# Kernel tuning notes

Hardware: AMD Instinct MI355X
Metric: run time of the kernel (lower is better)

The kernel has to match this reference:

```python
import jax, jax.numpy as jnp
import numpy as np

N_DIMS = 4          # len(dims): gauge-link channels split off by unpack_x
N_BANDS = 3         # SU(3) matrices
THRESHOLD = 1e-3    # trnorm_threshold
LAYER_CH = [6, 12, 12]  # input_channels + args.layer_channels


def cplx_einsum(eq, a, b):
    # complex einsum on real/imag-stacked tensors (last dim = 2)
    ar, ai = a[..., 0], a[..., 1]
    br, bi = b[..., 0], b[..., 1]
    re = jnp.einsum(eq, ar, br) - jnp.einsum(eq, ai, bi)
    im = jnp.einsum(eq, ar, bi) + jnp.einsum(eq, ai, br)
    return jnp.stack((re, im), axis=-1)


def h_conj(w):
    # hermitian conjugate: transpose matrix dims, negate imag part
    wt = jnp.swapaxes(w, -3, -2)
    return jnp.stack((wt[..., 0], -wt[..., 1]), axis=-1)


def gebl(x, weight):
    # x: [b, X, n_dims + n_in, nb, nb, 2]; weight: [n_out, w_in, w_in, 2]
    u, w = x[:, :, :N_DIMS], x[:, :, N_DIMS:]
    w = jnp.concatenate((w, h_conj(w)), axis=2)            # conjugation enlargement
    b, s = w.shape[0], w.shape[1]
    eye = jnp.zeros((N_BANDS, N_BANDS, 2), w.dtype).at[..., 0].set(jnp.eye(N_BANDS, dtype=w.dtype))
    unit = jnp.broadcast_to(eye, (b, s, 1, N_BANDS, N_BANDS, 2))
    w = jnp.concatenate((w, unit), axis=2)                 # unit elements
    ww = cplx_einsum('bxvij,bxwjk->bxvwik', w, w)          # pairwise matrix products
    w_out = cplx_einsum('uvw,bxvwij->bxuij', weight, ww)   # channel mixing
    return jnp.concatenate((u, w_out), axis=2)


def gerelu(x):
    u, w = x[:, :, :N_DIMS], x[:, :, N_DIMS:]
    tr_re = jnp.einsum('bxwiic->bxwc', w)[..., 0]          # Re(Tr W)
    w = jax.nn.relu(tr_re)[..., None, None, None] * w
    return jnp.concatenate((u, w), axis=2)


def trnorm(x):
    # trnorm_on_abs = True branch
    u, w = x[:, :, :N_DIMS], x[:, :, N_DIMS:]
    tr = jnp.einsum('bxviic->bxvc', w)
    tr_abs = jnp.sqrt(tr[..., 0] ** 2 + tr[..., 1] ** 2)
    norm = jnp.maximum(jnp.mean(tr_abs, axis=2), THRESHOLD)
    w = w / norm[:, :, None, None, None, None]
    return jnp.concatenate((u, w), axis=2)


def setup_inputs() -> dict:
    key = jax.random.key(0)
    ks = jax.random.split(key, 5)
    b, X = 2, 8 * 8 * 8 * 8
    x = jax.random.normal(ks[0], (b, X, N_DIMS + LAYER_CH[0], N_BANDS, N_BANDS, 2), jnp.float32)
    # GEBL weights: [n_out, w_in, w_in, 2], w_in = 2*n_in + 1
    w_in1 = 2 * LAYER_CH[0] + 1  # 13
    w_in2 = 2 * LAYER_CH[1] + 1  # 25
    w1 = jax.random.normal(ks[1], (LAYER_CH[1], w_in1, w_in1, 2), jnp.float32) * 0.1
    w2 = jax.random.normal(ks[2], (LAYER_CH[2], w_in2, w_in2, 2), jnp.float32) * 0.1
    dense_w = jax.random.normal(ks[3], (1, LAYER_CH[2] * 2), jnp.float32) * 0.2
    dense_b = jax.random.normal(ks[4], (1,), jnp.float32) * 0.01
    return {"x": x, "w1": w1, "w2": w2, "dense_w": dense_w, "dense_b": dense_b}


def reference(x, w1, w2, dense_w, dense_b):
    # GEBL -> GEReLU -> TrNorm (trnorm_before_ReLU=False), twice
    h = trnorm(gerelu(gebl(x, w1)))
    h = trnorm(gerelu(gebl(h, w2)))
    # Trace (normalized) -> reshape -> dense -> reshape
    w = h[:, :, N_DIMS:]
    tr = (1.0 / N_BANDS) * jnp.einsum('bxwiic->bxwc', w)   # [b, X, c, 2]
    flat = tr.reshape(-1, tr.shape[2] * 2)                 # torch .view: (c,2) interleaved
    out = flat @ dense_w.T + dense_b                        # [b*X, 1]
    return out.reshape(x.shape[0], -1)                      # [b, num_sites]
```

## Files before the change

kernel.cpp:

```cpp
#include <hip/hip_runtime.h>
#include <math.h>


#define NPTS 8192
#define THRESH 0.001f

__global__ void geblnet_setup(const float* __restrict__ w2,
                              float4* __restrict__ CTt) {
    int j = blockIdx.x * blockDim.x + threadIdx.x;
    if (j >= 12 * 169) return;
    int u = j / 169, it = j % 169;
    const float* W = w2 + u * 25 * 25 * 2;
#define WR(v, w) W[((v) * 25 + (w)) * 2]
#define WI(v, w) W[((v) * 25 + (w)) * 2 + 1]
    float c0, c1, c2, c3;
    if (it < 78) {
        int q = it, a = 0;
        while (q >= 12 - a) { q -= 12 - a; ++a; }
        int b = a + q;
        float ar = WR(a, b) + (a != b ? WR(b, a) : 0.f);
        float ai = WI(a, b) + (a != b ? WI(b, a) : 0.f);
        float br = WR(12 + a, 12 + b) + (a != b ? WR(12 + b, 12 + a) : 0.f);
        float bi = WI(12 + a, 12 + b) + (a != b ? WI(12 + b, 12 + a) : 0.f);
        c0 = ar + br; c1 = bi - ai; c2 = ai + bi; c3 = ar - br;
    } else if (it < 156) {
        int q = it - 78, a = 0;
        while (q >= 12 - a) { q -= 12 - a; ++a; }
        int b = a + q;
        if (a != b) {
            float gr = WR(a, 12 + b) + WR(12 + b, a);
            float gi = WI(a, 12 + b) + WI(12 + b, a);
            float dr = WR(b, 12 + a) + WR(12 + a, b);
            float di = WI(b, 12 + a) + WI(12 + a, b);
            c0 = gr + dr; c1 = di - gi; c2 = gi + di; c3 = gr - dr;
        } else {
            float er = WR(a, 12 + a) + WR(12 + a, a);
            float ei = WI(a, 12 + a) + WI(12 + a, a);
            c0 = er; c1 = 0.f; c2 = ei; c3 = 0.f;
        }
    } else if (it < 168) {
        int a = it - 156;
        float fr = WR(a, 24) + WR(24, a), fi = WI(a, 24) + WI(24, a);
        float pr = WR(12 + a, 24) + WR(24, 12 + a);
        float pi = WI(12 + a, 24) + WI(24, 12 + a);
        c0 = fr + pr; c1 = pi - fi; c2 = fi + pi; c3 = fr - pr;
    } else {
        c0 = 3.f * WR(24, 24); c1 = 0.f; c2 = 3.f * WI(24, 24); c3 = 0.f;
    }
    CTt[it * 12 + u] = make_float4(c0, c1, c2, c3);
#undef WR
#undef WI
}

__global__ __launch_bounds__(64) void geblnet_main(
    const float2* __restrict__ x2,
    const float2* __restrict__ w1g,
    const float* __restrict__ dw,
    const float* __restrict__ db,
    const float4* __restrict__ CTt,
    float* __restrict__ out)
{
    __shared__ float2 WeGV[170];
    __shared__ float2 Bs[780];
    __shared__ float2 Hs[108];
    __shared__ float2 Tpar[60];
    __shared__ float2 tr1[12];
    __shared__ float  sc1[12];
    __shared__ float  gb[12];
    __shared__ float  tra[12];

    const int t = threadIdx.x;
    const int p = blockIdx.x;

    for (int j = t; j < 117; j += 64) {
        int v = j / 9, ik = j - v * 9;
        int i = ik / 3, jj = ik - i * 3;
        float2 val;
        if (v < 6) val = x2[(size_t)p * 90 + (4 + v) * 9 + ik];
        else if (v < 12) {
            float2 s = x2[(size_t)p * 90 + (v - 2) * 9 + jj * 3 + i];
            val = make_float2(s.x, -s.y);
        } else val = make_float2((i == jj) ? 1.f : 0.f, 0.f);
        WeGV[v * 10 + ik] = val;
    }
    __syncthreads();

    #pragma unroll 1
    for (int g = 0; g < 2; ++g) {
        const int u0 = g * 6;
        #pragma unroll 1
        for (int e = t; e < 702; e += 64) {
            int uu = e / 117, rem = e - uu * 117;
            int v = rem / 9, jk = rem - v * 9;
            const float2* cp = w1g + ((u0 + uu) * 13 + v) * 13;
            float br = 0.f, bi = 0.f;
            #pragma unroll
            for (int w = 0; w < 13; ++w) {
                float2 cc = cp[w];
                float2 ee = WeGV[w * 10 + jk];
                br += cc.x * ee.x - cc.y * ee.y;
                bi += cc.x * ee.y + cc.y * ee.x;
            }
            Bs[(uu * 13 + v) * 10 + jk] = make_float2(br, bi);
        }
        __syncthreads();
        if (t < 54) {
            int uu = t / 9, ik = t - uu * 9;
            int i = ik / 3, k = ik - i * 3;
            float hr = 0.f, hi = 0.f;
            #pragma unroll
            for (int v = 0; v < 13; ++v) {
                const float2* a = &WeGV[v * 10 + i * 3];
                const float2* b = &Bs[(uu * 13 + v) * 10 + k];
                #pragma unroll
                for (int j = 0; j < 3; ++j) {
                    float2 aj = a[j];
                    float2 bj = b[j * 3];
                    hr += aj.x * bj.x - aj.y * bj.y;
                    hi += aj.x * bj.y + aj.y * bj.x;
                }
            }
            Hs[(u0 + uu) * 9 + ik] = make_float2(hr, hi);
        }
        __syncthreads();
    }

    if (t < 12) {
        float2 a = Hs[t * 9 + 0], b = Hs[t * 9 + 4], c = Hs[t * 9 + 8];
        float2 tt = make_float2(a.x + b.x + c.x, a.y + b.y + c.y);
        tr1[t] = tt;
        float gg = tt.x > 0.f ? tt.x : 0.f;
        gb[t] = gg;
        tra[t] = gg * sqrtf(tt.x * tt.x + tt.y * tt.y);
    }
    __syncthreads();
    if (t < 12) {
        float m = 0.f;
        #pragma unroll
        for (int u = 0; u < 12; ++u) m += tra[u];
        sc1[t] = gb[t] / fmaxf(m * (1.f / 12.f), THRESH);
    }
    __syncthreads();

    for (int it = t; it < 169; it += 64) {
        float2 val;
        if (it < 156) {
            int q = it < 78 ? it : it - 78;
            float fs = sqrtf(625.0f - 8.0f * (float)q);
            int a = (int)((25.0f - fs) * 0.5f);
            int b = q - (a * (25 - a)) / 2 + a;
            const float2* Ha = &Hs[a * 9];
            const float2* Hb = &Hs[b * 9];
            float s = sc1[a] * sc1[b];
            float vr = 0.f, vi = 0.f;
            if (it < 78) {
                #pragma unroll
                for (int i = 0; i < 3; ++i)
                    #pragma unroll
                    for (int jj = 0; jj < 3; ++jj) {
                        float2 A = Ha[i * 3 + jj], B = Hb[jj * 3 + i];
                        vr += A.x * B.x - A.y * B.y;
                        vi += A.x * B.y + A.y * B.x;
                    }
            } else {
                #pragma unroll
                for (int e = 0; e < 9; ++e) {
                    float2 A = Ha[e], B = Hb[e];
                    vr += A.x * B.x + A.y * B.y;
                    vi += A.y * B.x - A.x * B.y;
                }
            }
            val = make_float2(s * vr, s * vi);
        } else if (it < 168) {
            int a = it - 156;
            float s = sc1[a]; float2 tt = tr1[a];
            val = make_float2(s * tt.x, s * tt.y);
        } else {
            val = make_float2(1.f, 0.f);
        }
        WeGV[it] = val;
    }
    __syncthreads();

    if (t < 60) {
        int q = t / 12, u = t - q * 12;
        int i0 = q * 34, i1 = (q == 4) ? 169 : i0 + 34;
        float tre = 0.f, tim = 0.f;
        for (int it = i0; it < i1; ++it) {
            float4 c = CTt[it * 12 + u];
            float2 gv = WeGV[it];
            tre += c.x * gv.x + c.y * gv.y;
            tim += c.z * gv.x + c.w * gv.y;
        }
        Tpar[u * 5 + q] = make_float2(tre, tim);
    }
    __syncthreads();

    if (t < 12) {
        float2 tt = make_float2(0.f, 0.f);
        #pragma unroll
        for (int q = 0; q < 5; ++q) {
            float2 A = Tpar[t * 5 + q];
            tt.x += A.x; tt.y += A.y;
        }
        tr1[t] = tt;
        float g = tt.x > 0.f ? tt.x : 0.f;
        gb[t] = g;
        tra[t] = g * sqrtf(tt.x * tt.x + tt.y * tt.y);
    }
    __syncthreads();
    if (t == 0) {
        float m = 0.f;
        #pragma unroll
        for (int u = 0; u < 12; ++u) m += tra[u];
        float inv = 1.f / fmaxf(m * (1.f / 12.f), THRESH);
        float acc = db[0];
        #pragma unroll
        for (int u = 0; u < 12; ++u) {
            float s = gb[u] * inv * (1.f / 3.f);
            acc += s * (tr1[u].x * dw[2 * u] + tr1[u].y * dw[2 * u + 1]);
        }
        out[p] = acc;
    }
}

extern "C" void kernel_launch(void* const* d_in, const int* in_sizes, int n_in,
                              void* d_out, int out_size, void* d_ws, size_t ws_size,
                              hipStream_t stream) {
    const float* x  = (const float*)d_in[0];
    const float* w1 = (const float*)d_in[1];
    const float* w2 = (const float*)d_in[2];
    const float* dw = (const float*)d_in[3];
    const float* db = (const float*)d_in[4];
    float* outp = (float*)d_out;
    float4* CTt = (float4*)d_ws;

    geblnet_setup<<<(12 * 169 + 255) / 256, 256, 0, stream>>>(w2, CTt);

    geblnet_main<<<NPTS, 64, 0, stream>>>(
        (const float2*)x, (const float2*)w1, dw, db, CTt, outp);
}
```

Before: 134.7 us.

## Pack two sites per block, one wavefront each, replacing barriers with compiler fences

```diff
diff --git a/kernel.cpp b/kernel.cpp
--- a/kernel.cpp
+++ b/kernel.cpp
@@ -4,6 +4,7 @@
 
 #define NPTS 8192
 #define THRESH 0.001f
+#define WFENCE() asm volatile("" ::: "memory")
 
 __global__ void geblnet_setup(const float* __restrict__ w2,
                               float4* __restrict__ CTt) {
@@ -52,7 +53,7 @@
 #undef WI
 }
 
-__global__ __launch_bounds__(64) void geblnet_main(
+__global__ __launch_bounds__(128) void geblnet_main(
     const float2* __restrict__ x2,
     const float2* __restrict__ w1g,
     const float* __restrict__ dw,
@@ -60,19 +61,32 @@
     const float4* __restrict__ CTt,
     float* __restrict__ out)
 {
-    __shared__ float2 WeGV[170];
-    __shared__ float2 Bs[780];
-    __shared__ float2 Hs[108];
-    __shared__ float2 Tpar[60];
-    __shared__ float2 tr1[12];
-    __shared__ float  sc1[12];
-    __shared__ float  gb[12];
-    __shared__ float  tra[12];
+    __shared__ float2 WeGV_s[2 * 170];
+    __shared__ __align__(16) float2 WeT_s[2 * 126];
+    __shared__ float2 Bs_s[2 * 390];
+    __shared__ float2 Hs_s[2 * 108];
+    __shared__ float2 Tpar_s[2 * 60];
+    __shared__ float2 tr1_s[2 * 12];
+    __shared__ float  sc1_s[2 * 12];
+    __shared__ float  gb_s[2 * 12];
+    __shared__ float  tra_s[2 * 12];
 
     const int t = threadIdx.x;
-    const int p = blockIdx.x;
-
-    for (int j = t; j < 117; j += 64) {
+    const int wv = t >> 6;
+    const int l = t & 63;
+    const int p = blockIdx.x * 2 + wv;
+
+    float2* We  = &WeGV_s[wv * 170];
+    float2* WT  = &WeT_s[wv * 126];
+    float2* Bw  = &Bs_s[wv * 390];
+    float2* Hw  = &Hs_s[wv * 108];
+    float2* Tp  = &Tpar_s[wv * 60];
+    float2* tr1 = &tr1_s[wv * 12];
+    float*  sc1 = &sc1_s[wv * 12];
+    float*  gb  = &gb_s[wv * 12];
+    float*  tra = &tra_s[wv * 12];
+
+    for (int j = l; j < 117; j += 64) {
         int v = j / 9, ik = j - v * 9;
         int i = ik / 3, jj = ik - i * 3;
         float2 val;
@@ -81,37 +95,39 @@
             float2 s = x2[(size_t)p * 90 + (v - 2) * 9 + jj * 3 + i];
             val = make_float2(s.x, -s.y);
         } else val = make_float2((i == jj) ? 1.f : 0.f, 0.f);
-        WeGV[v * 10 + ik] = val;
-    }
-    __syncthreads();
+        We[v * 10 + ik] = val;
+        WT[ik * 14 + v] = val;
+    }
+    WFENCE();
 
     #pragma unroll 1
-    for (int g = 0; g < 2; ++g) {
-        const int u0 = g * 6;
+    for (int g = 0; g < 4; ++g) {
+        const int u0 = g * 3;
         #pragma unroll 1
-        for (int e = t; e < 702; e += 64) {
+        for (int e = l; e < 351; e += 64) {
             int uu = e / 117, rem = e - uu * 117;
             int v = rem / 9, jk = rem - v * 9;
             const float2* cp = w1g + ((u0 + uu) * 13 + v) * 13;
+            const float2* wt = &WT[jk * 14];
             float br = 0.f, bi = 0.f;
             #pragma unroll
             for (int w = 0; w < 13; ++w) {
                 float2 cc = cp[w];
-                float2 ee = WeGV[w * 10 + jk];
+                float2 ee = wt[w];
                 br += cc.x * ee.x - cc.y * ee.y;
                 bi += cc.x * ee.y + cc.y * ee.x;
             }
-            Bs[(uu * 13 + v) * 10 + jk] = make_float2(br, bi);
-        }
-        __syncthreads();
-        if (t < 54) {
-            int uu = t / 9, ik = t - uu * 9;
+            Bw[(uu * 13 + v) * 10 + jk] = make_float2(br, bi);
+        }
+        WFENCE();
+        if (l < 27) {
+            int uu = l / 9, ik = l - uu * 9;
             int i = ik / 3, k = ik - i * 3;
             float hr = 0.f, hi = 0.f;
             #pragma unroll
             for (int v = 0; v < 13; ++v) {
-                const float2* a = &WeGV[v * 10 + i * 3];
-                const float2* b = &Bs[(uu * 13 + v) * 10 + k];
+                const float2* a = &We[v * 10 + i * 3];
+                const float2* b = &Bw[(uu * 13 + v) * 10 + k];
                 #pragma unroll
                 for (int j = 0; j < 3; ++j) {
                     float2 aj = a[j];
@@ -120,37 +136,37 @@
                     hi += aj.x * bj.y + aj.y * bj.x;
                 }
             }
-            Hs[(u0 + uu) * 9 + ik] = make_float2(hr, hi);
-        }
-        __syncthreads();
-    }
-
-    if (t < 12) {
-        float2 a = Hs[t * 9 + 0], b = Hs[t * 9 + 4], c = Hs[t * 9 + 8];
+            Hw[(u0 + uu) * 9 + ik] = make_float2(hr, hi);
+        }
+        WFENCE();
+    }
+
+    if (l < 12) {
+        float2 a = Hw[l * 9 + 0], b = Hw[l * 9 + 4], c = Hw[l * 9 + 8];
         float2 tt = make_float2(a.x + b.x + c.x, a.y + b.y + c.y);
-        tr1[t] = tt;
+        tr1[l] = tt;
         float gg = tt.x > 0.f ? tt.x : 0.f;
-        gb[t] = gg;
-        tra[t] = gg * sqrtf(tt.x * tt.x + tt.y * tt.y);
-    }
-    __syncthreads();
-    if (t < 12) {
+        gb[l] = gg;
+        tra[l] = gg * sqrtf(tt.x * tt.x + tt.y * tt.y);
+    }
+    WFENCE();
+    if (l < 12) {
         float m = 0.f;
         #pragma unroll
         for (int u = 0; u < 12; ++u) m += tra[u];
-        sc1[t] = gb[t] / fmaxf(m * (1.f / 12.f), THRESH);
-    }
-    __syncthreads();
-
-    for (int it = t; it < 169; it += 64) {
+        sc1[l] = gb[l] / fmaxf(m * (1.f / 12.f), THRESH);
+    }
+    WFENCE();
+
+    for (int it = l; it < 169; it += 64) {
         float2 val;
         if (it < 156) {
             int q = it < 78 ? it : it - 78;
             float fs = sqrtf(625.0f - 8.0f * (float)q);
             int a = (int)((25.0f - fs) * 0.5f);
             int b = q - (a * (25 - a)) / 2 + a;
-            const float2* Ha = &Hs[a * 9];
-            const float2* Hb = &Hs[b * 9];
+            const float2* Ha = &Hw[a * 9];
+            const float2* Hb = &Hw[b * 9];
             float s = sc1[a] * sc1[b];
             float vr = 0.f, vi = 0.f;
             if (it < 78) {
@@ -178,38 +194,38 @@
         } else {
             val = make_float2(1.f, 0.f);
         }
-        WeGV[it] = val;
-    }
-    __syncthreads();
-
-    if (t < 60) {
-        int q = t / 12, u = t - q * 12;
+        We[it] = val;
+    }
+    WFENCE();
+
+    if (l < 60) {
+        int q = l / 12, u = l - q * 12;
         int i0 = q * 34, i1 = (q == 4) ? 169 : i0 + 34;
         float tre = 0.f, tim = 0.f;
         for (int it = i0; it < i1; ++it) {
             float4 c = CTt[it * 12 + u];
-            float2 gv = WeGV[it];
+            float2 gv = We[it];
             tre += c.x * gv.x + c.y * gv.y;
             tim += c.z * gv.x + c.w * gv.y;
         }
-        Tpar[u * 5 + q] = make_float2(tre, tim);
-    }
-    __syncthreads();
-
-    if (t < 12) {
+        Tp[u * 5 + q] = make_float2(tre, tim);
+    }
+    WFENCE();
+
+    if (l < 12) {
         float2 tt = make_float2(0.f, 0.f);
         #pragma unroll
         for (int q = 0; q < 5; ++q) {
-            float2 A = Tpar[t * 5 + q];
+            float2 A = Tp[l * 5 + q];
             tt.x += A.x; tt.y += A.y;
         }
-        tr1[t] = tt;
+        tr1[l] = tt;
         float g = tt.x > 0.f ? tt.x : 0.f;
-        gb[t] = g;
-        tra[t] = g * sqrtf(tt.x * tt.x + tt.y * tt.y);
-    }
-    __syncthreads();
-    if (t == 0) {
+        gb[l] = g;
+        tra[l] = g * sqrtf(tt.x * tt.x + tt.y * tt.y);
+    }
+    WFENCE();
+    if (l == 0) {
         float m = 0.f;
         #pragma unroll
         for (int u = 0; u < 12; ++u) m += tra[u];
@@ -237,6 +253,6 @@
 
     geblnet_setup<<<(12 * 169 + 255) / 256, 256, 0, stream>>>(w2, CTt);
 
-    geblnet_main<<<NPTS, 64, 0, stream>>>(
+    geblnet_main<<<NPTS / 2, 128, 0, stream>>>(
         (const float2*)x, (const float2*)w1, dw, db, CTt, outp);
 }
```

Result: slower. 139.9 us (+3.9%).
